# Kernel optimization log

Hardware: AMD Instinct MI355X
Metric: run time of the kernel (lower is better)

The kernel has to match this reference:

```python
import jax, jax.numpy as jnp
import numpy as np


def setup_inputs() -> dict:
    key = jax.random.key(0)
    k1, k2 = jax.random.split(key)
    x = jax.random.normal(k1, (8, 64, 256, 256), dtype=jnp.float32)
    grid = jax.random.normal(k2, (8, 256, 256, 2), dtype=jnp.float32)
    return {"x": x, "grid": grid}


def _warp_bilinear_zeros(x, grid):
    # x: [N, C, H, W]; grid: [N, Ho, Wo, 2] with (dx, dy) pixel offsets.
    N, C, H, W = x.shape
    Ho, Wo = grid.shape[1], grid.shape[2]
    dt = grid.dtype
    base_y = jnp.arange(Ho, dtype=dt)[:, None]   # [Ho, 1]
    base_x = jnp.arange(Wo, dtype=dt)[None, :]   # [1, Wo]
    abs_x = grid[..., 0] + base_x                # [N, Ho, Wo]
    abs_y = grid[..., 1] + base_y
    # normalize then unnormalize (align_corners=True), matching the torch chain
    norm_x = abs_x * 2 / (W - 1) - 1
    norm_y = abs_y * 2 / (H - 1) - 1
    ix = (norm_x + 1) * 0.5 * (W - 1)
    iy = (norm_y + 1) * 0.5 * (H - 1)

    x0 = jnp.floor(ix); x1 = x0 + 1
    y0 = jnp.floor(iy); y1 = y0 + 1
    wx1 = ix - x0; wx0 = 1 - wx1
    wy1 = iy - y0; wy0 = 1 - wy1

    inb_x0 = (x0 >= 0) & (x0 <= W - 1)
    inb_x1 = (x1 >= 0) & (x1 <= W - 1)
    inb_y0 = (y0 >= 0) & (y0 <= H - 1)
    inb_y1 = (y1 >= 0) & (y1 <= H - 1)

    xi0 = jnp.clip(x0, 0, W - 1).astype(jnp.int32)
    xi1 = jnp.clip(x1, 0, W - 1).astype(jnp.int32)
    yi0 = jnp.clip(y0, 0, H - 1).astype(jnp.int32)
    yi1 = jnp.clip(y1, 0, H - 1).astype(jnp.int32)

    def gather(img, yi, xi):  # img [C,H,W], yi/xi [Ho,Wo] -> [C,Ho,Wo]
        return img[:, yi, xi]
    g = jax.vmap(gather)

    # zeros padding: mask out-of-bounds corner contributions
    w00 = (wy0 * wx0 * (inb_y0 & inb_x0).astype(dt))[:, None]  # [N,1,Ho,Wo]
    w01 = (wy0 * wx1 * (inb_y0 & inb_x1).astype(dt))[:, None]
    w10 = (wy1 * wx0 * (inb_y1 & inb_x0).astype(dt))[:, None]
    w11 = (wy1 * wx1 * (inb_y1 & inb_x1).astype(dt))[:, None]

    out = (g(x, yi0, xi0) * w00 + g(x, yi0, xi1) * w01
           + g(x, yi1, xi0) * w10 + g(x, yi1, xi1) * w11)
    return out  # [N, C, Ho, Wo]


def reference(x, grid):
    return _warp_bilinear_zeros(x, grid)
```

## Files before the change

kernel.cpp:

```cpp
#include <hip/hip_runtime.h>


#define N_ 8
#define C_ 64
#define H_ 256
#define W_ 256
#define HO_ 256
#define WO_ 256
#define CCH 8
#define NCC (C_ / CCH)
#define RMAX 12
#define LDSW 260

__global__ __launch_bounds__(256) void gridsample_kernel(
    const float* __restrict__ x,
    const float2* __restrict__ grid2,
    float* __restrict__ out)
{
    __shared__ __attribute__((aligned(16))) float sm[2][RMAX * LDSW];
    __shared__ int swin[8];

    const int b     = blockIdx.x;
    const int xcd   = b & 7;
    const int idx   = b >> 3;
    const int plane = xcd * (NCC * N_ / 8) + (idx >> 8);
    const int ho    = idx & 255;
    const int n     = plane >> 3;
    const int cc    = plane & 7;
    const int wo    = threadIdx.x;
    const int ln    = threadIdx.x & 63;
    const int wv    = threadIdx.x >> 6;

    const int sp = (n * HO_ + ho) * WO_ + wo;
    const float2 g = grid2[sp];

    const float absx = g.x + (float)wo;
    const float absy = g.y + (float)ho;
    const float normx = absx * 2.0f / (float)(W_ - 1) - 1.0f;
    const float normy = absy * 2.0f / (float)(H_ - 1) - 1.0f;
    const float ix = (normx + 1.0f) * 0.5f * (float)(W_ - 1);
    const float iy = (normy + 1.0f) * 0.5f * (float)(H_ - 1);

    const float x0f = floorf(ix);
    const float y0f = floorf(iy);
    const float x1f = x0f + 1.0f;
    const float y1f = y0f + 1.0f;

    const float wx1 = ix - x0f, wx0 = 1.0f - wx1;
    const float wy1 = iy - y0f, wy0 = 1.0f - wy1;

    const float hx0 = ((x0f >= 0.0f) && (x0f <= (float)(W_ - 1))) ? wx0 : 0.0f;
    const float hx1 = ((x1f >= 0.0f) && (x1f <= (float)(W_ - 1))) ? wx1 : 0.0f;
    const float ey0 = ((y0f >= 0.0f) && (y0f <= (float)(H_ - 1))) ? wy0 : 0.0f;
    const float ey1 = ((y1f >= 0.0f) && (y1f <= (float)(H_ - 1))) ? wy1 : 0.0f;

    const int xlo = (int)fminf(fmaxf(x0f, 0.0f), (float)(W_ - 2));
    const bool hi = (x0f >= (float)(W_ - 1));
    const bool lo = (x0f <= -1.0f);
    const float A = (hi ? 0.0f : hx0) + (lo ? hx1 : 0.0f);
    const float B = (hi ? hx0 : 0.0f) + (lo ? 0.0f : hx1);

    const float W00 = A * ey0, W01 = B * ey0;
    const float W10 = A * ey1, W11 = B * ey1;

    const int yr0 = min(max((int)y0f, 0), H_ - 1);
    const int yr1 = min(max((int)y1f, 0), H_ - 1);

    int lmin = yr0, lmax = yr1;
    #pragma unroll
    for (int m = 32; m >= 1; m >>= 1) {
        lmin = min(lmin, __shfl_xor(lmin, m));
        lmax = max(lmax, __shfl_xor(lmax, m));
    }
    if (ln == 0) { swin[wv] = lmin; swin[4 + wv] = lmax; }
    __syncthreads();
    const int wlo  = min(min(swin[0], swin[1]), min(swin[2], swin[3]));
    const int whi0 = max(max(swin[4], swin[5]), max(swin[6], swin[7]));
    const int whi  = min(whi0, wlo + RMAX - 1);
    const int R    = whi - wlo + 1;

    const int o0 = min(yr0 - wlo, RMAX - 1) * LDSW + xlo;
    const int o1 = min(yr1 - wlo, RMAX - 1) * LDSW + xlo;
    const bool oow0 = yr0 > whi;
    const bool oow1 = yr1 > whi;
    const int r0 = yr0 * W_ + xlo;
    const int r1 = yr1 * W_ + xlo;

    const int c0 = cc * CCH;
    const float* __restrict__ xb =
        x + ((size_t)n * C_ + c0) * (H_ * W_);
    float* __restrict__ ob =
        out + (((size_t)n * C_ + c0) * HO_ + ho) * WO_ + wo;

    for (int r = wv; r < R; r += 4) {
        const float* gp = xb + (size_t)(wlo + r) * W_ + ln * 4;
        __builtin_amdgcn_global_load_lds(
            (const __attribute__((address_space(1))) void*)gp,
            (__attribute__((address_space(3))) void*)&sm[0][r * LDSW],
            16, 0, 0);
    }
    __syncthreads();

    #pragma unroll
    for (int c = 0; c < CCH; ++c) {
        if (c + 1 < CCH) {
            const float* xn = xb + (size_t)(c + 1) * (H_ * W_);
            for (int r = wv; r < R; r += 4) {
                const float* gp = xn + (size_t)(wlo + r) * W_ + ln * 4;
                __builtin_amdgcn_global_load_lds(
                    (const __attribute__((address_space(1))) void*)gp,
                    (__attribute__((address_space(3))) void*)&sm[(c + 1) & 1][r * LDSW],
                    16, 0, 0);
            }
        }

        const float* smb = sm[c & 1];
        float p00 = smb[o0];
        float p01 = smb[o0 + 1];
        float p10 = smb[o1];
        float p11 = smb[o1 + 1];

        if (__builtin_expect(oow0, 0)) {
            const float* xc = xb + (size_t)c * (H_ * W_);
            p00 = xc[r0];
            p01 = xc[r0 + 1];
        }
        if (__builtin_expect(oow1, 0)) {
            const float* xc = xb + (size_t)c * (H_ * W_);
            p10 = xc[r1];
            p11 = xc[r1 + 1];
        }

        ob[(size_t)c * (HO_ * WO_)] =
            p00 * W00 + p01 * W01 + p10 * W10 + p11 * W11;

        if (c + 1 < CCH) __syncthreads();
    }
}

extern "C" void kernel_launch(void* const* d_in, const int* in_sizes, int n_in,
                              void* d_out, int out_size, void* d_ws, size_t ws_size,
                              hipStream_t stream) {
    const float*  x    = (const float*)d_in[0];
    const float2* grid = (const float2*)d_in[1];
    float*        out  = (float*)d_out;

    const int nblocks = N_ * NCC * HO_;
    gridsample_kernel<<<nblocks, 256, 0, stream>>>(x, grid, out);
}
```

Before: 291.8 us.

## Process two output rows per block sharing one staged input row window

Each block now handles two consecutive output rows. They share a single LDS window of input rows, which grows from 12 to 15 rows, and the grid halves. Because adjacent output rows sample overlapping input rows, this cuts redundant global-to-LDS loads and halves the per-block fixed overhead. In exchange each block loads a larger window, uses more LDS and registers, and has fewer blocks to spread across the GPU.

```diff
diff --git a/kernel.cpp b/kernel.cpp
--- a/kernel.cpp
+++ b/kernel.cpp
@@ -9,7 +9,8 @@
 #define WO_ 256
 #define CCH 8
 #define NCC (C_ / CCH)
-#define RMAX 12
+#define HB 2
+#define RMAX 15
 #define LDSW 260
 
 __global__ __launch_bounds__(256) void gridsample_kernel(
@@ -23,50 +24,63 @@
     const int b     = blockIdx.x;
     const int xcd   = b & 7;
     const int idx   = b >> 3;
-    const int plane = xcd * (NCC * N_ / 8) + (idx >> 8);
-    const int ho    = idx & 255;
+    const int plane = xcd * (NCC * N_ / 8) + (idx >> 7);
+    const int ho2   = (idx & 127) * HB;
     const int n     = plane >> 3;
     const int cc    = plane & 7;
     const int wo    = threadIdx.x;
     const int ln    = threadIdx.x & 63;
     const int wv    = threadIdx.x >> 6;
 
-    const int sp = (n * HO_ + ho) * WO_ + wo;
-    const float2 g = grid2[sp];
+    float W00[HB], W01[HB], W10[HB], W11[HB];
+    int   o0[HB], o1[HB], r0[HB], r1[HB];
+    bool  oow0[HB], oow1[HB];
+    int   yr0[HB], yr1[HB];
+    int   xlo[HB];
 
-    const float absx = g.x + (float)wo;
-    const float absy = g.y + (float)ho;
-    const float normx = absx * 2.0f / (float)(W_ - 1) - 1.0f;
-    const float normy = absy * 2.0f / (float)(H_ - 1) - 1.0f;
-    const float ix = (normx + 1.0f) * 0.5f * (float)(W_ - 1);
-    const float iy = (normy + 1.0f) * 0.5f * (float)(H_ - 1);
+    int lmin = H_, lmax = -1;
 
-    const float x0f = floorf(ix);
-    const float y0f = floorf(iy);
-    const float x1f = x0f + 1.0f;
-    const float y1f = y0f + 1.0f;
+    #pragma unroll
+    for (int j = 0; j < HB; ++j) {
+        const int ho = ho2 + j;
+        const int sp = (n * HO_ + ho) * WO_ + wo;
+        const float2 g = grid2[sp];
 
-    const float wx1 = ix - x0f, wx0 = 1.0f - wx1;
-    const float wy1 = iy - y0f, wy0 = 1.0f - wy1;
+        const float absx = g.x + (float)wo;
+        const float absy = g.y + (float)ho;
+        const float normx = absx * 2.0f / (float)(W_ - 1) - 1.0f;
+        const float normy = absy * 2.0f / (float)(H_ - 1) - 1.0f;
+        const float ix = (normx + 1.0f) * 0.5f * (float)(W_ - 1);
+        const float iy = (normy + 1.0f) * 0.5f * (float)(H_ - 1);
 
-    const float hx0 = ((x0f >= 0.0f) && (x0f <= (float)(W_ - 1))) ? wx0 : 0.0f;
-    const float hx1 = ((x1f >= 0.0f) && (x1f <= (float)(W_ - 1))) ? wx1 : 0.0f;
-    const float ey0 = ((y0f >= 0.0f) && (y0f <= (float)(H_ - 1))) ? wy0 : 0.0f;
-    const float ey1 = ((y1f >= 0.0f) && (y1f <= (float)(H_ - 1))) ? wy1 : 0.0f;
+        const float x0f = floorf(ix);
+        const float y0f = floorf(iy);
+        const float x1f = x0f + 1.0f;
+        const float y1f = y0f + 1.0f;
 
-    const int xlo = (int)fminf(fmaxf(x0f, 0.0f), (float)(W_ - 2));
-    const bool hi = (x0f >= (float)(W_ - 1));
-    const bool lo = (x0f <= -1.0f);
-    const float A = (hi ? 0.0f : hx0) + (lo ? hx1 : 0.0f);
-    const float B = (hi ? hx0 : 0.0f) + (lo ? 0.0f : hx1);
+        const float wx1 = ix - x0f, wx0 = 1.0f - wx1;
+        const float wy1 = iy - y0f, wy0 = 1.0f - wy1;
 
-    const float W00 = A * ey0, W01 = B * ey0;
-    const float W10 = A * ey1, W11 = B * ey1;
+        const float hx0 = ((x0f >= 0.0f) && (x0f <= (float)(W_ - 1))) ? wx0 : 0.0f;
+        const float hx1 = ((x1f >= 0.0f) && (x1f <= (float)(W_ - 1))) ? wx1 : 0.0f;
+        const float ey0 = ((y0f >= 0.0f) && (y0f <= (float)(H_ - 1))) ? wy0 : 0.0f;
+        const float ey1 = ((y1f >= 0.0f) && (y1f <= (float)(H_ - 1))) ? wy1 : 0.0f;
 
-    const int yr0 = min(max((int)y0f, 0), H_ - 1);
-    const int yr1 = min(max((int)y1f, 0), H_ - 1);
+        xlo[j] = (int)fminf(fmaxf(x0f, 0.0f), (float)(W_ - 2));
+        const bool hi = (x0f >= (float)(W_ - 1));
+        const bool lo = (x0f <= -1.0f);
+        const float A = (hi ? 0.0f : hx0) + (lo ? hx1 : 0.0f);
+        const float B = (hi ? hx0 : 0.0f) + (lo ? 0.0f : hx1);
 
-    int lmin = yr0, lmax = yr1;
+        W00[j] = A * ey0; W01[j] = B * ey0;
+        W10[j] = A * ey1; W11[j] = B * ey1;
+
+        yr0[j] = min(max((int)y0f, 0), H_ - 1);
+        yr1[j] = min(max((int)y1f, 0), H_ - 1);
+        lmin = min(lmin, yr0[j]);
+        lmax = max(lmax, yr1[j]);
+    }
+
     #pragma unroll
     for (int m = 32; m >= 1; m >>= 1) {
         lmin = min(lmin, __shfl_xor(lmin, m));
@@ -79,18 +93,21 @@
     const int whi  = min(whi0, wlo + RMAX - 1);
     const int R    = whi - wlo + 1;
 
-    const int o0 = min(yr0 - wlo, RMAX - 1) * LDSW + xlo;
-    const int o1 = min(yr1 - wlo, RMAX - 1) * LDSW + xlo;
-    const bool oow0 = yr0 > whi;
-    const bool oow1 = yr1 > whi;
-    const int r0 = yr0 * W_ + xlo;
-    const int r1 = yr1 * W_ + xlo;
+    #pragma unroll
+    for (int j = 0; j < HB; ++j) {
+        o0[j] = min(yr0[j] - wlo, RMAX - 1) * LDSW + xlo[j];
+        o1[j] = min(yr1[j] - wlo, RMAX - 1) * LDSW + xlo[j];
+        oow0[j] = yr0[j] > whi;
+        oow1[j] = yr1[j] > whi;
+        r0[j] = yr0[j] * W_ + xlo[j];
+        r1[j] = yr1[j] * W_ + xlo[j];
+    }
 
     const int c0 = cc * CCH;
     const float* __restrict__ xb =
         x + ((size_t)n * C_ + c0) * (H_ * W_);
     float* __restrict__ ob =
-        out + (((size_t)n * C_ + c0) * HO_ + ho) * WO_ + wo;
+        out + (((size_t)n * C_ + c0) * HO_ + ho2) * WO_ + wo;
 
     for (int r = wv; r < R; r += 4) {
         const float* gp = xb + (size_t)(wlo + r) * W_ + ln * 4;
@@ -115,24 +132,27 @@
         }
 
         const float* smb = sm[c & 1];
-        float p00 = smb[o0];
-        float p01 = smb[o0 + 1];
-        float p10 = smb[o1];
-        float p11 = smb[o1 + 1];
+        const float* __restrict__ xc = xb + (size_t)c * (H_ * W_);
 
-        if (__builtin_expect(oow0, 0)) {
-            const float* xc = xb + (size_t)c * (H_ * W_);
-            p00 = xc[r0];
-            p01 = xc[r0 + 1];
+        #pragma unroll
+        for (int j = 0; j < HB; ++j) {
+            float p00 = smb[o0[j]];
+            float p01 = smb[o0[j] + 1];
+            float p10 = smb[o1[j]];
+            float p11 = smb[o1[j] + 1];
+
+            if (__builtin_expect(oow0[j], 0)) {
+                p00 = xc[r0[j]];
+                p01 = xc[r0[j] + 1];
+            }
+            if (__builtin_expect(oow1[j], 0)) {
+                p10 = xc[r1[j]];
+                p11 = xc[r1[j] + 1];
+            }
+
+            ob[(size_t)c * (HO_ * WO_) + (size_t)j * WO_] =
+                p00 * W00[j] + p01 * W01[j] + p10 * W10[j] + p11 * W11[j];
         }
-        if (__builtin_expect(oow1, 0)) {
-            const float* xc = xb + (size_t)c * (H_ * W_);
-            p10 = xc[r1];
-            p11 = xc[r1 + 1];
-        }
-
-        ob[(size_t)c * (HO_ * WO_)] =
-            p00 * W00 + p01 * W01 + p10 * W10 + p11 * W11;
 
         if (c + 1 < CCH) __syncthreads();
     }
@@ -145,6 +165,6 @@
     const float2* grid = (const float2*)d_in[1];
     float*        out  = (float*)d_out;
 
-    const int nblocks = N_ * NCC * HO_;
+    const int nblocks = N_ * NCC * (HO_ / HB);
     gridsample_kernel<<<nblocks, 256, 0, stream>>>(x, grid, out);
 }
```

Measured after the change: 279.5 us. 1.04x faster.
